# Kernel optimization log

Hardware: AMD Instinct MI355X
Metric: run time of the kernel (lower is better)

The kernel has to match this reference:

```python
import jax, jax.numpy as jnp
import numpy as np


def _lstm(x, Wih, Whh, bih, bhh):
    # x: (T, B, F); Wih: (4H, F); Whh: (4H, H); torch gate order i, f, g, o
    T, B, _ = x.shape
    H = Whh.shape[1]
    # precompute input projections for all timesteps (one big GEMM)
    xg = jnp.einsum('tbf,gf->tbg', x, Wih) + bih + bhh  # (T, B, 4H)

    def step(carry, gx):
        h, c = carry
        g = gx + h @ Whh.T  # (B, 4H)
        i, f, gg, o = jnp.split(g, 4, axis=-1)
        i = jax.nn.sigmoid(i)
        f = jax.nn.sigmoid(f)
        gg = jnp.tanh(gg)
        o = jax.nn.sigmoid(o)
        c = f * c + i * gg
        h = o * jnp.tanh(c)
        return (h, c), h

    h0 = jnp.zeros((B, H), x.dtype)
    (_, _), out = jax.lax.scan(step, (h0, h0), xg)
    return out  # (T, B, H)


def setup_inputs() -> dict:
    key = jax.random.key(0)
    ks = jax.random.split(key, 20)
    T, B, F = 1024, 512, 32
    H1, H2, H3 = 32, 8, 8  # lstm1 hidden=32, lstm2 hidden=8, lstm3 hidden=out_features=8
    p = 0.25
    s = 0.1  # weight init scale

    def mk_mask(k, h):
        keep = (jax.random.uniform(k, (B, h)) > p).astype(jnp.float32)
        return keep / (1.0 - p)

    return {
        'x': jax.random.normal(ks[0], (T, B, F), jnp.float32),
        'W_ih1': jax.random.normal(ks[1], (4 * H1, F)) * s,
        'W_hh1': jax.random.normal(ks[2], (4 * H1, H1)) * s,
        'b_ih1': jax.random.normal(ks[3], (4 * H1,)) * s,
        'b_hh1': jax.random.normal(ks[4], (4 * H1,)) * s,
        'W_ih2': jax.random.normal(ks[5], (4 * H2, H1)) * s,
        'W_hh2': jax.random.normal(ks[6], (4 * H2, H2)) * s,
        'b_ih2': jax.random.normal(ks[7], (4 * H2,)) * s,
        'b_hh2': jax.random.normal(ks[8], (4 * H2,)) * s,
        'W_ih3': jax.random.normal(ks[9], (4 * H3, H2)) * s,
        'W_hh3': jax.random.normal(ks[10], (4 * H3, H3)) * s,
        'b_ih3': jax.random.normal(ks[11], (4 * H3,)) * s,
        'b_hh3': jax.random.normal(ks[12], (4 * H3,)) * s,
        'mask1': mk_mask(ks[13], H1),
        'mask2': mk_mask(ks[14], H2),
        'mask3': mk_mask(ks[15], H3),
    }


def reference(x, W_ih1, W_hh1, b_ih1, b_hh1,
              W_ih2, W_hh2, b_ih2, b_hh2,
              W_ih3, W_hh3, b_ih3, b_hh3,
              mask1, mask2, mask3):
    # Locked (variational) output dropout: one mask per sequence, broadcast over time.
    out = _lstm(x, W_ih1, W_hh1, b_ih1, b_hh1) * mask1[None, :, :]
    out = _lstm(out, W_ih2, W_hh2, b_ih2, b_hh2) * mask2[None, :, :]
    out = _lstm(out, W_ih3, W_hh3, b_ih3, b_hh3) * mask3[None, :, :]
    return out  # (T, B, out_features)
```

## Files before the change

### kernel.cpp

```cpp
#include <hip/hip_runtime.h>


constexpr int T = 1024, B = 512, F = 32;
constexpr int H1 = 32, H2 = 8, H3 = 8;
constexpr int G1 = 4 * H1;
constexpr int HR = 128;
constexpr int XR = 64;
constexpr int OUT_STRIDE = B * H3;

typedef float f32x2 __attribute__((ext_vector_type(2)));
typedef unsigned int u32x2 __attribute__((ext_vector_type(2)));

#define PIN(v) asm volatile("" : "+v"(v))

#if __has_builtin(__builtin_amdgcn_rcpf)
#define RCPF(x) __builtin_amdgcn_rcpf(x)
#else
#define RCPF(x) (1.0f / (x))
#endif
#if __has_builtin(__builtin_amdgcn_exp2f)
#define EXP2F(x) __builtin_amdgcn_exp2f(x)
#else
#define EXP2F(x) exp2f(x)
#endif

#if __has_builtin(__builtin_amdgcn_permlane32_swap)
#define HAVE_PLSWAP 1
#else
#define HAVE_PLSWAP 0
#endif

#define SIG_CM (-1.4426950408889634f)

__device__ __forceinline__ void pkfma(f32x2& acc, f32x2 a, f32x2 b) {
    acc += a * b;
}

#define LDS_ACQ(p)    __hip_atomic_load((p), __ATOMIC_ACQUIRE, __HIP_MEMORY_SCOPE_WORKGROUP)
#define LDS_REL(p, v) __hip_atomic_store((p), (v), __ATOMIC_RELEASE, __HIP_MEMORY_SCOPE_WORKGROUP)
#define SPIN_UNTIL(EXPR)                                                       \
    do {                                                                       \
        int _g = 0;                                                            \
        while (!(EXPR)) {                                                      \
            __builtin_amdgcn_s_sleep(1);                                       \
            if (++_g > (1 << 23)) break;                                       \
        }                                                                      \
    } while (0)

__global__ __launch_bounds__(192, 1) void lstm3_fused_kernel(
    const float* __restrict__ x,
    const float* __restrict__ Wih1, const float* __restrict__ Whh1,
    const float* __restrict__ bih1, const float* __restrict__ bhh1,
    const float* __restrict__ Wih2, const float* __restrict__ Whh2,
    const float* __restrict__ bih2, const float* __restrict__ bhh2,
    const float* __restrict__ Wih3, const float* __restrict__ Whh3,
    const float* __restrict__ bih3, const float* __restrict__ bhh3,
    const float* __restrict__ mask1, const float* __restrict__ mask2,
    const float* __restrict__ mask3,
    float* __restrict__ out)
{
    const int tid = threadIdx.x;
    const int lane = tid & 63;
    const int wid = tid >> 6;
    const int b = blockIdx.x;

    __shared__ __align__(16) float h1ring[HR][H1];
    __shared__ __align__(16) float xgring[XR][G1];
    __shared__ __align__(16) float xstage[32][F];
    __shared__ __align__(16) float sh23[2][16];
    __shared__ int prog0, prog1, prog2;

    if (tid == 0) { prog0 = 0; prog1 = 0; prog2 = 0; }
    if (wid == 0 && lane < H1) h1ring[HR - 1][lane] = 0.f;
    if (wid == 1 && lane < 16) { sh23[0][lane] = 0.f; sh23[1][lane] = 0.f; }
    __syncthreads();

    if (wid == 2) {
        const float cmA = SIG_CM;
        const float cmB = (lane < 32) ? 2.0f * SIG_CM : SIG_CM;
        f32x2 wi0[16], wi1[16];
#pragma unroll
        for (int k = 0; k < 16; ++k) {
            wi0[k] = f32x2{Wih1[lane * F + 2 * k] * cmA, Wih1[lane * F + 2 * k + 1] * cmA};
            wi1[k] = f32x2{Wih1[(lane + 64) * F + 2 * k] * cmB, Wih1[(lane + 64) * F + 2 * k + 1] * cmB};
        }
        const float bias0 = (bih1[lane] + bhh1[lane]) * cmA;
        const float bias1 = (bih1[lane + 64] + bhh1[lane + 64]) * cmB;
#pragma unroll
        for (int k = 0; k < 16; ++k) { PIN(wi0[k]); PIN(wi1[k]); }

        const float4* x4 = (const float4*)x;
        float4* xr4 = (float4*)xstage;
        const int ttq = lane >> 3, ffq = lane & 7;

        float4 sA = x4[(size_t)(0 + ttq) * 4096 + b * 8 + ffq];
        float4 sB = x4[(size_t)(8 + ttq) * 4096 + b * 8 + ffq];
        xr4[(ttq & 31) * 8 + ffq] = sA;
        xr4[((8 + ttq) & 31) * 8 + ffq] = sB;
        sA = x4[(size_t)(16 + ttq) * 4096 + b * 8 + ffq];
        sB = x4[(size_t)(24 + ttq) * 4096 + b * 8 + ffq];

        for (int t = 0; t < T; ++t) {
            if ((t & 15) == 0) {
                const int need = t - 40;
                if (need > 0) SPIN_UNTIL(LDS_ACQ(&prog0) >= need);
                const int wt = t + 16;
                if (wt < T) {
                    xr4[((wt + ttq) & 31) * 8 + ffq] = sA;
                    xr4[((wt + 8 + ttq) & 31) * 8 + ffq] = sB;
                    const int lt = t + 32;
                    if (lt < T) {
                        sA = x4[(size_t)(lt + ttq) * 4096 + b * 8 + ffq];
                        sB = x4[(size_t)(lt + 8 + ttq) * 4096 + b * 8 + ffq];
                    }
                }
            }
            const float4* xp = (const float4*)xstage[t & 31];
            f32x2 aA = f32x2{bias0, 0.f}, aB = f32x2{0.f, 0.f};
            f32x2 cA = f32x2{bias1, 0.f}, cB = f32x2{0.f, 0.f};
#pragma unroll
            for (int q = 0; q < 8; ++q) {
                const float4 v = xp[q];
                const f32x2 lo = f32x2{v.x, v.y}, hi = f32x2{v.z, v.w};
                pkfma(aA, wi0[2 * q], lo); pkfma(aB, wi0[2 * q + 1], hi);
                pkfma(cA, wi1[2 * q], lo); pkfma(cB, wi1[2 * q + 1], hi);
            }
            const f32x2 sa = aA + aB, sc = cA + cB;
            xgring[t & (XR - 1)][lane] = sa.x + sa.y;
            xgring[t & (XR - 1)][lane + 64] = sc.x + sc.y;
            if ((t & 15) == 15) LDS_REL(&prog2, t + 1);
        }
    } else if (wid == 0) {
        const float s1d = 2.0f * SIG_CM;
        const float cm1 = (lane < 32) ? 2.0f * SIG_CM : SIG_CM;
        f32x2 w0[16], w1[16];
#pragma unroll
        for (int k = 0; k < 16; ++k) {
            w0[k] = f32x2{Whh1[lane * H1 + 2 * k] * SIG_CM, Whh1[lane * H1 + 2 * k + 1] * SIG_CM};
            w1[k] = f32x2{Whh1[(lane + 64) * H1 + 2 * k] * cm1, Whh1[(lane + 64) * H1 + 2 * k + 1] * cm1};
        }
#pragma unroll
        for (int k = 0; k < 16; ++k) { PIN(w0[k]); PIN(w1[k]); }
        const float ka1 = (lane < 32) ? (s1d + s1d) : 1.0f;
        const float kb1 = (lane < 32) ? -s1d : 0.0f;
        float c1s = 0.f;

        SPIN_UNTIL(LDS_ACQ(&prog2) >= ((34 < T) ? 34 : T));
        float pa = xgring[0][lane], pb = xgring[0][lane + 64];
        float na = xgring[1][lane], nb = xgring[1][lane + 64];

        for (int i = 0; i < T; ++i) {
            if ((i & 31) == 0 && i) {
                int tgt = i + 34; if (tgt > T) tgt = T;
                SPIN_UNTIL(LDS_ACQ(&prog2) >= tgt);
            }
            if ((i & 63) == 0 && i >= 64)
                SPIN_UNTIL(LDS_ACQ(&prog1) >= i - 48);

            const float4* h1p = (const float4*)h1ring[(i - 1) & (HR - 1)];
            f32x2 hp2[16];
#pragma unroll
            for (int q = 0; q < 8; ++q) {
                const float4 v = h1p[q];
                hp2[2 * q] = f32x2{v.x, v.y};
                hp2[2 * q + 1] = f32x2{v.z, v.w};
            }
            f32x2 A0 = f32x2{pa, 0.f}, A1 = f32x2{0.f, 0.f};
            f32x2 A2 = f32x2{0.f, 0.f}, A3 = f32x2{0.f, 0.f};
            f32x2 B0 = f32x2{pb, 0.f}, B1 = f32x2{0.f, 0.f};
            f32x2 B2 = f32x2{0.f, 0.f}, B3 = f32x2{0.f, 0.f};
#pragma unroll
            for (int d = 0; d < 4; ++d) {
                pkfma(A0, w0[0 + 4 * d], hp2[0 + 4 * d]);
                pkfma(A1, w0[1 + 4 * d], hp2[1 + 4 * d]);
                pkfma(A2, w0[2 + 4 * d], hp2[2 + 4 * d]);
                pkfma(A3, w0[3 + 4 * d], hp2[3 + 4 * d]);
                pkfma(B0, w1[0 + 4 * d], hp2[0 + 4 * d]);
                pkfma(B1, w1[1 + 4 * d], hp2[1 + 4 * d]);
                pkfma(B2, w1[2 + 4 * d], hp2[2 + 4 * d]);
                pkfma(B3, w1[3 + 4 * d], hp2[3 + 4 * d]);
            }
            const f32x2 SA = (A0 + A1) + (A2 + A3);
            const f32x2 SB = (B0 + B1) + (B2 + B3);
            const float a0s = SA.x + SA.y;
            const float a1s = SB.x + SB.y;
            const float g0 = RCPF(1.0f + EXP2F(a0s));
            const float g1 = fmaf(ka1, RCPF(1.0f + EXP2F(a1s)), kb1);
            pa = na; pb = nb;
            {
                int tn = i + 2; if (tn > T - 1) tn = T - 1;
                na = xgring[tn & (XR - 1)][lane];
                nb = xgring[tn & (XR - 1)][lane + 64];
            }
            float h1v;
#if HAVE_PLSWAP
            const u32x2 pif = __builtin_amdgcn_permlane32_swap(
                __float_as_uint(g0), __float_as_uint(g0), false, false);
            const u32x2 pgo = __builtin_amdgcn_permlane32_swap(
                __float_as_uint(g1), __float_as_uint(g1), false, false);
            const float iv = __uint_as_float(pif.x);
            const float fv = __uint_as_float(pif.y);
            const float gsv = __uint_as_float(pgo.x);
            const float ov = __uint_as_float(pgo.y);
            c1s = fmaf(fv, c1s, iv * gsv);
            const float rt = RCPF(1.0f + EXP2F(c1s));
            h1v = fmaf(ov + ov, rt, -ov);
#else
            const float fv = __shfl_xor(g0, 32);
            const float ov = __shfl_xor(g1, 32);
            c1s = fmaf(fv, c1s, g0 * g1);
            const float rt = RCPF(1.0f + EXP2F(c1s));
            h1v = fmaf(ov + ov, rt, -ov);
#endif
            if (lane < H1) h1ring[i & (HR - 1)][lane] = h1v;
            if ((i & 7) == 7) LDS_REL(&prog0, i + 1);
        }
    } else {
        const float sX = 2.0f * SIG_CM;
        const int r = lane & 31;
        const bool lower = (lane < 32);
        const int sec = r >> 3;
        const float cmX = (sec == 2) ? sX : SIG_CM;
        const float kaX = (sec == 2) ? (sX + sX) : 1.0f;
        const float kbX = (sec == 2) ? -sX : 0.0f;
        f32x2 wp[16];
        f32x2 wup[8];
        float biasX, m3;
        if (lower) {
#pragma unroll
            for (int k = 0; k < 16; ++k)
                wp[k] = f32x2{Wih2[r * H1 + 2 * k] * mask1[b * H1 + 2 * k] * cmX,
                              Wih2[r * H1 + 2 * k + 1] * mask1[b * H1 + 2 * k + 1] * cmX};
#pragma unroll
            for (int k = 0; k < 4; ++k)
                wup[k] = f32x2{Whh2[r * H2 + 2 * k] * cmX, Whh2[r * H2 + 2 * k + 1] * cmX};
#pragma unroll
            for (int k = 0; k < 4; ++k) wup[4 + k] = f32x2{0.f, 0.f};
            biasX = (bih2[r] + bhh2[r]) * cmX;
        } else {
#pragma unroll
            for (int k = 0; k < 16; ++k) wp[k] = f32x2{0.f, 0.f};
#pragma unroll
            for (int k = 0; k < 4; ++k)
                wup[k] = f32x2{Wih3[r * H2 + 2 * k] * mask2[b * H2 + 2 * k] * cmX,
                               Wih3[r * H2 + 2 * k + 1] * mask2[b * H2 + 2 * k + 1] * cmX};
#pragma unroll
            for (int k = 0; k < 4; ++k)
                wup[4 + k] = f32x2{Whh3[r * H3 + 2 * k] * cmX, Whh3[r * H3 + 2 * k + 1] * cmX};
            biasX = (bih3[r] + bhh3[r]) * cmX;
        }
        m3 = mask3[b * H3 + (lane & 7)];
        const int thresh = lower ? 1 : 2;
        const int gbase = (lane & 32) + (lane & 7);
        const int bx0 = 4 * (gbase + 0),  bx1 = 4 * (gbase + 8);
        const int bx2 = 4 * (gbase + 16), bx3 = 4 * (gbase + 24);
#pragma unroll
        for (int k = 0; k < 16; ++k) PIN(wp[k]);
#pragma unroll
        for (int k = 0; k < 8; ++k) PIN(wup[k]);

        float c23s = 0.f;
        f32x2 hq2[16];
        {
            const float4* hp0 = (const float4*)h1ring[HR - 1];
#pragma unroll
            for (int q = 0; q < 8; ++q) {
                const float4 v = hp0[q];
                hq2[2 * q] = f32x2{v.x, v.y};
                hq2[2 * q + 1] = f32x2{v.z, v.w};
            }
        }

        for (int i = 0; i <= T + 1; ++i) {
            if ((i & 7) == 0) {
                int tgt = i + 8; if (tgt > T) tgt = T;
                SPIN_UNTIL(LDS_ACQ(&prog0) >= tgt);
            }
            const int par = i & 1;
            const float4* up = (const float4*)sh23[par ^ 1];
            const float4 u0 = up[0], u1 = up[1], u2 = up[2], u3 = up[3];
            f32x2 S0 = f32x2{biasX, 0.f}, S1 = f32x2{0.f, 0.f};
            f32x2 S2 = f32x2{0.f, 0.f}, S3 = f32x2{0.f, 0.f};
#pragma unroll
            for (int d = 0; d < 4; ++d) {
                pkfma(S0, wp[0 + 4 * d], hq2[0 + 4 * d]);
                pkfma(S1, wp[1 + 4 * d], hq2[1 + 4 * d]);
                pkfma(S2, wp[2 + 4 * d], hq2[2 + 4 * d]);
                pkfma(S3, wp[3 + 4 * d], hq2[3 + 4 * d]);
            }
            f32x2 U0 = f32x2{0.f, 0.f}, U1 = f32x2{0.f, 0.f};
            f32x2 U2 = f32x2{0.f, 0.f}, U3 = f32x2{0.f, 0.f};
            pkfma(U0, wup[0], f32x2{u0.x, u0.y}); pkfma(U0, wup[4], f32x2{u2.x, u2.y});
            pkfma(U1, wup[1], f32x2{u0.z, u0.w}); pkfma(U1, wup[5], f32x2{u2.z, u2.w});
            pkfma(U2, wup[2], f32x2{u1.x, u1.y}); pkfma(U2, wup[6], f32x2{u3.x, u3.y});
            pkfma(U3, wup[3], f32x2{u1.z, u1.w}); pkfma(U3, wup[7], f32x2{u3.z, u3.w});
            const f32x2 ST = ((S0 + S1) + (S2 + S3)) + ((U0 + U1) + (U2 + U3));
            const float a23s = ST.x + ST.y;
            const float rv = fmaf(kaX, RCPF(1.0f + EXP2F(a23s)), kbX);
            float gi, gf, gg, go;
            asm volatile(
                "ds_bpermute_b32 %0, %4, %8\n\t"
                "ds_bpermute_b32 %1, %5, %8\n\t"
                "ds_bpermute_b32 %2, %6, %8\n\t"
                "ds_bpermute_b32 %3, %7, %8\n\t"
                "s_waitcnt lgkmcnt(0)"
                : "=&v"(gi), "=&v"(gf), "=&v"(gg), "=&v"(go)
                : "v"(bx0), "v"(bx1), "v"(bx2), "v"(bx3), "v"(rv)
                : "memory");
            {
                const float4* hp = (const float4*)h1ring[i & (HR - 1)];
#pragma unroll
                for (int q = 0; q < 8; ++q) {
                    const float4 v = hp[q];
                    hq2[2 * q] = f32x2{v.x, v.y};
                    hq2[2 * q + 1] = f32x2{v.z, v.w};
                }
            }
            c23s = (i >= thresh) ? fmaf(gf, c23s, gi * gg) : 0.0f;
            const float rt = RCPF(1.0f + EXP2F(c23s));
            const float hnew = fmaf(go + go, rt, -go);
            if (i >= 2 && (lane & 56) == 32)
                out[(size_t)(i - 2) * OUT_STRIDE + b * H3 + (lane & 7)] = hnew * m3;
            if ((lane & 24) == 0)
                sh23[par][(lane & 7) | ((lane & 32) >> 2)] = hnew;
            if ((i & 15) == 15) LDS_REL(&prog1, i + 1);
        }
    }
}

extern "C" void kernel_launch(void* const* d_in, const int* in_sizes, int n_in,
                              void* d_out, int out_size, void* d_ws, size_t ws_size,
                              hipStream_t stream) {
    (void)in_sizes; (void)n_in; (void)out_size; (void)d_ws; (void)ws_size;
    const float* x     = (const float*)d_in[0];
    const float* Wih1  = (const float*)d_in[1];
    const float* Whh1  = (const float*)d_in[2];
    const float* bih1  = (const float*)d_in[3];
    const float* bhh1  = (const float*)d_in[4];
    const float* Wih2  = (const float*)d_in[5];
    const float* Whh2  = (const float*)d_in[6];
    const float* bih2  = (const float*)d_in[7];
    const float* bhh2  = (const float*)d_in[8];
    const float* Wih3  = (const float*)d_in[9];
    const float* Whh3  = (const float*)d_in[10];
    const float* bih3  = (const float*)d_in[11];
    const float* bhh3  = (const float*)d_in[12];
    const float* mask1 = (const float*)d_in[13];
    const float* mask2 = (const float*)d_in[14];
    const float* mask3 = (const float*)d_in[15];
    float* out = (float*)d_out;

    lstm3_fused_kernel<<<dim3(B), dim3(192), 0, stream>>>(
        x, Wih1, Whh1, bih1, bhh1,
        Wih2, Whh2, bih2, bhh2,
        Wih3, Whh3, bih3, bhh3,
        mask1, mask2, mask3, out);
}
```

Measured before the change: 507.6 us.

## Process two batch sequences per block to interleave independent LSTM recurrences

Each block now handles two batch elements instead of one, with every wave running two independent recurrence chains interleaved in the same loop, and the grid halved. This is meant to hide the latency of the serial per-timestep dependency chain (LDS reads, exp/rcp, lane swaps, bpermute) by giving the scheduler independent work, and to halve the number of blocks on the device. It roughly doubles register pressure and removes the PIN register-pinning asm barriers, so spills or a worse schedule are possible. With 256 blocks on a part that has at least that many CUs, the per-block serial chain gets longer while total parallel width shrinks.

```diff
diff --git a/kernel.cpp b/kernel.cpp
--- a/kernel.cpp
+++ b/kernel.cpp
@@ -10,8 +10,6 @@
 
 typedef float f32x2 __attribute__((ext_vector_type(2)));
 typedef unsigned int u32x2 __attribute__((ext_vector_type(2)));
-
-#define PIN(v) asm volatile("" : "+v"(v))
 
 #if __has_builtin(__builtin_amdgcn_rcpf)
 #define RCPF(x) __builtin_amdgcn_rcpf(x)
@@ -62,17 +60,24 @@
     const int tid = threadIdx.x;
     const int lane = tid & 63;
     const int wid = tid >> 6;
-    const int b = blockIdx.x;
-
-    __shared__ __align__(16) float h1ring[HR][H1];
-    __shared__ __align__(16) float xgring[XR][G1];
-    __shared__ __align__(16) float xstage[32][F];
-    __shared__ __align__(16) float sh23[2][16];
+    const int b0 = 2 * blockIdx.x;
+    const int b1 = b0 + 1;
+
+    __shared__ __align__(16) float h1ring[2][HR][H1];
+    __shared__ __align__(16) float xgring[2][XR][G1];
+    __shared__ __align__(16) float xstage[2][32][F];
+    __shared__ __align__(16) float sh23[2][2][16];
     __shared__ int prog0, prog1, prog2;
 
     if (tid == 0) { prog0 = 0; prog1 = 0; prog2 = 0; }
-    if (wid == 0 && lane < H1) h1ring[HR - 1][lane] = 0.f;
-    if (wid == 1 && lane < 16) { sh23[0][lane] = 0.f; sh23[1][lane] = 0.f; }
+    if (wid == 0 && lane < H1) {
+        h1ring[0][HR - 1][lane] = 0.f;
+        h1ring[1][HR - 1][lane] = 0.f;
+    }
+    if (wid == 1 && lane < 16) {
+        sh23[0][0][lane] = 0.f; sh23[0][1][lane] = 0.f;
+        sh23[1][0][lane] = 0.f; sh23[1][1][lane] = 0.f;
+    }
     __syncthreads();
 
     if (wid == 2) {
@@ -86,19 +91,24 @@
         }
         const float bias0 = (bih1[lane] + bhh1[lane]) * cmA;
         const float bias1 = (bih1[lane + 64] + bhh1[lane + 64]) * cmB;
-#pragma unroll
-        for (int k = 0; k < 16; ++k) { PIN(wi0[k]); PIN(wi1[k]); }
 
         const float4* x4 = (const float4*)x;
-        float4* xr4 = (float4*)xstage;
+        float4* xr0 = (float4*)xstage[0];
+        float4* xr1 = (float4*)xstage[1];
         const int ttq = lane >> 3, ffq = lane & 7;
 
-        float4 sA = x4[(size_t)(0 + ttq) * 4096 + b * 8 + ffq];
-        float4 sB = x4[(size_t)(8 + ttq) * 4096 + b * 8 + ffq];
-        xr4[(ttq & 31) * 8 + ffq] = sA;
-        xr4[((8 + ttq) & 31) * 8 + ffq] = sB;
-        sA = x4[(size_t)(16 + ttq) * 4096 + b * 8 + ffq];
-        sB = x4[(size_t)(24 + ttq) * 4096 + b * 8 + ffq];
+        float4 sA0 = x4[(size_t)(0 + ttq) * 4096 + b0 * 8 + ffq];
+        float4 sB0 = x4[(size_t)(8 + ttq) * 4096 + b0 * 8 + ffq];
+        float4 sA1 = x4[(size_t)(0 + ttq) * 4096 + b1 * 8 + ffq];
+        float4 sB1 = x4[(size_t)(8 + ttq) * 4096 + b1 * 8 + ffq];
+        xr0[(ttq & 31) * 8 + ffq] = sA0;
+        xr0[((8 + ttq) & 31) * 8 + ffq] = sB0;
+        xr1[(ttq & 31) * 8 + ffq] = sA1;
+        xr1[((8 + ttq) & 31) * 8 + ffq] = sB1;
+        sA0 = x4[(size_t)(16 + ttq) * 4096 + b0 * 8 + ffq];
+        sB0 = x4[(size_t)(24 + ttq) * 4096 + b0 * 8 + ffq];
+        sA1 = x4[(size_t)(16 + ttq) * 4096 + b1 * 8 + ffq];
+        sB1 = x4[(size_t)(24 + ttq) * 4096 + b1 * 8 + ffq];
 
         for (int t = 0; t < T; ++t) {
             if ((t & 15) == 0) {
@@ -106,28 +116,41 @@
                 if (need > 0) SPIN_UNTIL(LDS_ACQ(&prog0) >= need);
                 const int wt = t + 16;
                 if (wt < T) {
-                    xr4[((wt + ttq) & 31) * 8 + ffq] = sA;
-                    xr4[((wt + 8 + ttq) & 31) * 8 + ffq] = sB;
+                    xr0[((wt + ttq) & 31) * 8 + ffq] = sA0;
+                    xr0[((wt + 8 + ttq) & 31) * 8 + ffq] = sB0;
+                    xr1[((wt + ttq) & 31) * 8 + ffq] = sA1;
+                    xr1[((wt + 8 + ttq) & 31) * 8 + ffq] = sB1;
                     const int lt = t + 32;
                     if (lt < T) {
-                        sA = x4[(size_t)(lt + ttq) * 4096 + b * 8 + ffq];
-                        sB = x4[(size_t)(lt + 8 + ttq) * 4096 + b * 8 + ffq];
+                        sA0 = x4[(size_t)(lt + ttq) * 4096 + b0 * 8 + ffq];
+                        sB0 = x4[(size_t)(lt + 8 + ttq) * 4096 + b0 * 8 + ffq];
+                        sA1 = x4[(size_t)(lt + ttq) * 4096 + b1 * 8 + ffq];
+                        sB1 = x4[(size_t)(lt + 8 + ttq) * 4096 + b1 * 8 + ffq];
                     }
                 }
             }
-            const float4* xp = (const float4*)xstage[t & 31];
-            f32x2 aA = f32x2{bias0, 0.f}, aB = f32x2{0.f, 0.f};
-            f32x2 cA = f32x2{bias1, 0.f}, cB = f32x2{0.f, 0.f};
+            const float4* xp0 = (const float4*)xstage[0][t & 31];
+            const float4* xp1 = (const float4*)xstage[1][t & 31];
+            f32x2 aA0 = f32x2{bias0, 0.f}, aB0 = f32x2{0.f, 0.f};
+            f32x2 cA0 = f32x2{bias1, 0.f}, cB0 = f32x2{0.f, 0.f};
+            f32x2 aA1 = f32x2{bias0, 0.f}, aB1 = f32x2{0.f, 0.f};
+            f32x2 cA1 = f32x2{bias1, 0.f}, cB1 = f32x2{0.f, 0.f};
 #pragma unroll
             for (int q = 0; q < 8; ++q) {
-                const float4 v = xp[q];
-                const f32x2 lo = f32x2{v.x, v.y}, hi = f32x2{v.z, v.w};
-                pkfma(aA, wi0[2 * q], lo); pkfma(aB, wi0[2 * q + 1], hi);
-                pkfma(cA, wi1[2 * q], lo); pkfma(cB, wi1[2 * q + 1], hi);
-            }
-            const f32x2 sa = aA + aB, sc = cA + cB;
-            xgring[t & (XR - 1)][lane] = sa.x + sa.y;
-            xgring[t & (XR - 1)][lane + 64] = sc.x + sc.y;
+                const float4 v0 = xp0[q], v1 = xp1[q];
+                const f32x2 lo0 = f32x2{v0.x, v0.y}, hi0 = f32x2{v0.z, v0.w};
+                const f32x2 lo1 = f32x2{v1.x, v1.y}, hi1 = f32x2{v1.z, v1.w};
+                pkfma(aA0, wi0[2 * q], lo0); pkfma(aB0, wi0[2 * q + 1], hi0);
+                pkfma(cA0, wi1[2 * q], lo0); pkfma(cB0, wi1[2 * q + 1], hi0);
+                pkfma(aA1, wi0[2 * q], lo1); pkfma(aB1, wi0[2 * q + 1], hi1);
+                pkfma(cA1, wi1[2 * q], lo1); pkfma(cB1, wi1[2 * q + 1], hi1);
+            }
+            const f32x2 sa0 = aA0 + aB0, sc0 = cA0 + cB0;
+            const f32x2 sa1 = aA1 + aB1, sc1 = cA1 + cB1;
+            xgring[0][t & (XR - 1)][lane] = sa0.x + sa0.y;
+            xgring[0][t & (XR - 1)][lane + 64] = sc0.x + sc0.y;
+            xgring[1][t & (XR - 1)][lane] = sa1.x + sa1.y;
+            xgring[1][t & (XR - 1)][lane + 64] = sc1.x + sc1.y;
             if ((t & 15) == 15) LDS_REL(&prog2, t + 1);
         }
     } else if (wid == 0) {
@@ -139,15 +162,15 @@
             w0[k] = f32x2{Whh1[lane * H1 + 2 * k] * SIG_CM, Whh1[lane * H1 + 2 * k + 1] * SIG_CM};
             w1[k] = f32x2{Whh1[(lane + 64) * H1 + 2 * k] * cm1, Whh1[(lane + 64) * H1 + 2 * k + 1] * cm1};
         }
-#pragma unroll
-        for (int k = 0; k < 16; ++k) { PIN(w0[k]); PIN(w1[k]); }
         const float ka1 = (lane < 32) ? (s1d + s1d) : 1.0f;
         const float kb1 = (lane < 32) ? -s1d : 0.0f;
-        float c1s = 0.f;
+        float c1s_0 = 0.f, c1s_1 = 0.f;
 
         SPIN_UNTIL(LDS_ACQ(&prog2) >= ((34 < T) ? 34 : T));
-        float pa = xgring[0][lane], pb = xgring[0][lane + 64];
-        float na = xgring[1][lane], nb = xgring[1][lane + 64];
+        float pa0 = xgring[0][0][lane], pb0 = xgring[0][0][lane + 64];
+        float na0 = xgring[0][1][lane], nb0 = xgring[0][1][lane + 64];
+        float pa1 = xgring[1][0][lane], pb1 = xgring[1][0][lane + 64];
+        float na1 = xgring[1][1][lane], nb1 = xgring[1][1][lane + 64];
 
         for (int i = 0; i < T; ++i) {
             if ((i & 31) == 0 && i) {
@@ -157,62 +180,111 @@
             if ((i & 63) == 0 && i >= 64)
                 SPIN_UNTIL(LDS_ACQ(&prog1) >= i - 48);
 
-            const float4* h1p = (const float4*)h1ring[(i - 1) & (HR - 1)];
-            f32x2 hp2[16];
+            const float4* h1p0 = (const float4*)h1ring[0][(i - 1) & (HR - 1)];
+            const float4* h1p1 = (const float4*)h1ring[1][(i - 1) & (HR - 1)];
+            f32x2 hp0[16], hp1[16];
 #pragma unroll
             for (int q = 0; q < 8; ++q) {
-                const float4 v = h1p[q];
-                hp2[2 * q] = f32x2{v.x, v.y};
-                hp2[2 * q + 1] = f32x2{v.z, v.w};
-            }
-            f32x2 A0 = f32x2{pa, 0.f}, A1 = f32x2{0.f, 0.f};
-            f32x2 A2 = f32x2{0.f, 0.f}, A3 = f32x2{0.f, 0.f};
-            f32x2 B0 = f32x2{pb, 0.f}, B1 = f32x2{0.f, 0.f};
-            f32x2 B2 = f32x2{0.f, 0.f}, B3 = f32x2{0.f, 0.f};
+                const float4 v = h1p0[q];
+                hp0[2 * q] = f32x2{v.x, v.y};
+                hp0[2 * q + 1] = f32x2{v.z, v.w};
+            }
+#pragma unroll
+            for (int q = 0; q < 8; ++q) {
+                const float4 v = h1p1[q];
+                hp1[2 * q] = f32x2{v.x, v.y};
+                hp1[2 * q + 1] = f32x2{v.z, v.w};
+            }
+            f32x2 A00 = f32x2{pa0, 0.f}, A01 = f32x2{0.f, 0.f};
+            f32x2 A02 = f32x2{0.f, 0.f}, A03 = f32x2{0.f, 0.f};
+            f32x2 B00 = f32x2{pb0, 0.f}, B01 = f32x2{0.f, 0.f};
+            f32x2 B02 = f32x2{0.f, 0.f}, B03 = f32x2{0.f, 0.f};
+            f32x2 A10 = f32x2{pa1, 0.f}, A11 = f32x2{0.f, 0.f};
+            f32x2 A12 = f32x2{0.f, 0.f}, A13 = f32x2{0.f, 0.f};
+            f32x2 B10 = f32x2{pb1, 0.f}, B11 = f32x2{0.f, 0.f};
+            f32x2 B12 = f32x2{0.f, 0.f}, B13 = f32x2{0.f, 0.f};
 #pragma unroll
             for (int d = 0; d < 4; ++d) {
-                pkfma(A0, w0[0 + 4 * d], hp2[0 + 4 * d]);
-                pkfma(A1, w0[1 + 4 * d], hp2[1 + 4 * d]);
-                pkfma(A2, w0[2 + 4 * d], hp2[2 + 4 * d]);
-                pkfma(A3, w0[3 + 4 * d], hp2[3 + 4 * d]);
-                pkfma(B0, w1[0 + 4 * d], hp2[0 + 4 * d]);
-                pkfma(B1, w1[1 + 4 * d], hp2[1 + 4 * d]);
-                pkfma(B2, w1[2 + 4 * d], hp2[2 + 4 * d]);
-                pkfma(B3, w1[3 + 4 * d], hp2[3 + 4 * d]);
-            }
-            const f32x2 SA = (A0 + A1) + (A2 + A3);
-            const f32x2 SB = (B0 + B1) + (B2 + B3);
-            const float a0s = SA.x + SA.y;
-            const float a1s = SB.x + SB.y;
-            const float g0 = RCPF(1.0f + EXP2F(a0s));
-            const float g1 = fmaf(ka1, RCPF(1.0f + EXP2F(a1s)), kb1);
-            pa = na; pb = nb;
+                pkfma(A00, w0[0 + 4 * d], hp0[0 + 4 * d]);
+                pkfma(A01, w0[1 + 4 * d], hp0[1 + 4 * d]);
+                pkfma(A02, w0[2 + 4 * d], hp0[2 + 4 * d]);
+                pkfma(A03, w0[3 + 4 * d], hp0[3 + 4 * d]);
+                pkfma(B00, w1[0 + 4 * d], hp0[0 + 4 * d]);
+                pkfma(B01, w1[1 + 4 * d], hp0[1 + 4 * d]);
+                pkfma(B02, w1[2 + 4 * d], hp0[2 + 4 * d]);
+                pkfma(B03, w1[3 + 4 * d], hp0[3 + 4 * d]);
+            }
+#pragma unroll
+            for (int d = 0; d < 4; ++d) {
+                pkfma(A10, w0[0 + 4 * d], hp1[0 + 4 * d]);
+                pkfma(A11, w0[1 + 4 * d], hp1[1 + 4 * d]);
+                pkfma(A12, w0[2 + 4 * d], hp1[2 + 4 * d]);
+                pkfma(A13, w0[3 + 4 * d], hp1[3 + 4 * d]);
+                pkfma(B10, w1[0 + 4 * d], hp1[0 + 4 * d]);
+                pkfma(B11, w1[1 + 4 * d], hp1[1 + 4 * d]);
+                pkfma(B12, w1[2 + 4 * d], hp1[2 + 4 * d]);
+                pkfma(B13, w1[3 + 4 * d], hp1[3 + 4 * d]);
+            }
+            const f32x2 SA0 = (A00 + A01) + (A02 + A03);
+            const f32x2 SB0 = (B00 + B01) + (B02 + B03);
+            const f32x2 SA1 = (A10 + A11) + (A12 + A13);
+            const f32x2 SB1 = (B10 + B11) + (B12 + B13);
+            const float g0_0 = RCPF(1.0f + EXP2F(SA0.x + SA0.y));
+            const float g1_0 = fmaf(ka1, RCPF(1.0f + EXP2F(SB0.x + SB0.y)), kb1);
+            const float g0_1 = RCPF(1.0f + EXP2F(SA1.x + SA1.y));
+            const float g1_1 = fmaf(ka1, RCPF(1.0f + EXP2F(SB1.x + SB1.y)), kb1);
+            pa0 = na0; pb0 = nb0; pa1 = na1; pb1 = nb1;
             {
                 int tn = i + 2; if (tn > T - 1) tn = T - 1;
-                na = xgring[tn & (XR - 1)][lane];
-                nb = xgring[tn & (XR - 1)][lane + 64];
-            }
-            float h1v;
+                na0 = xgring[0][tn & (XR - 1)][lane];
+                nb0 = xgring[0][tn & (XR - 1)][lane + 64];
+                na1 = xgring[1][tn & (XR - 1)][lane];
+                nb1 = xgring[1][tn & (XR - 1)][lane + 64];
+            }
+            float h1v0, h1v1;
 #if HAVE_PLSWAP
-            const u32x2 pif = __builtin_amdgcn_permlane32_swap(
-                __float_as_uint(g0), __float_as_uint(g0), false, false);
-            const u32x2 pgo = __builtin_amdgcn_permlane32_swap(
-                __float_as_uint(g1), __float_as_uint(g1), false, false);
-            const float iv = __uint_as_float(pif.x);
-            const float fv = __uint_as_float(pif.y);
-            const float gsv = __uint_as_float(pgo.x);
-            const float ov = __uint_as_float(pgo.y);
-            c1s = fmaf(fv, c1s, iv * gsv);
-            const float rt = RCPF(1.0f + EXP2F(c1s));
-            h1v = fmaf(ov + ov, rt, -ov);
+            {
+                const u32x2 pif = __builtin_amdgcn_permlane32_swap(
+                    __float_as_uint(g0_0), __float_as_uint(g0_0), false, false);
+                const u32x2 pgo = __builtin_amdgcn_permlane32_swap(
+                    __float_as_uint(g1_0), __float_as_uint(g1_0), false, false);
+                c1s_0 = fmaf(__uint_as_float(pif.y), c1s_0,
+                             __uint_as_float(pif.x) * __uint_as_float(pgo.x));
+                const float rt = RCPF(1.0f + EXP2F(c1s_0));
+                const float ov = __uint_as_float(pgo.y);
+                h1v0 = fmaf(ov + ov, rt, -ov);
+            }
+            {
+                const u32x2 pif = __builtin_amdgcn_permlane32_swap(
+                    __float_as_uint(g0_1), __float_as_uint(g0_1), false, false);
+                const u32x2 pgo = __builtin_amdgcn_permlane32_swap(
+                    __float_as_uint(g1_1), __float_as_uint(g1_1), false, false);
+                c1s_1 = fmaf(__uint_as_float(pif.y), c1s_1,
+                             __uint_as_float(pif.x) * __uint_as_float(pgo.x));
+                const float rt = RCPF(1.0f + EXP2F(c1s_1));
+                const float ov = __uint_as_float(pgo.y);
+                h1v1 = fmaf(ov + ov, rt, -ov);
+            }
 #else
-            const float fv = __shfl_xor(g0, 32);
-            const float ov = __shfl_xor(g1, 32);
-            c1s = fmaf(fv, c1s, g0 * g1);
-            const float rt = RCPF(1.0f + EXP2F(c1s));
-            h1v = fmaf(ov + ov, rt, -ov);
+            {
+                const float fv = __shfl_xor(g0_0, 32);
+                const float ov = __shfl_xor(g1_0, 32);
+                c1s_0 = fmaf(fv, c1s_0, g0_0 * g1_0);
+                const float rt = RCPF(1.0f + EXP2F(c1s_0));
+                h1v0 = fmaf(ov + ov, rt, -ov);
+            }
+            {
+                const float fv = __shfl_xor(g0_1, 32);
+                const float ov = __shfl_xor(g1_1, 32);
+                c1s_1 = fmaf(fv, c1s_1, g0_1 * g1_1);
+                const float rt = RCPF(1.0f + EXP2F(c1s_1));
+                h1v1 = fmaf(ov + ov, rt, -ov);
+            }
 #endif
-            if (lane < H1) h1ring[i & (HR - 1)][lane] = h1v;
+            if (lane < H1) {
+                h1ring[0][i & (HR - 1)][lane] = h1v0;
+                h1ring[1][i & (HR - 1)][lane] = h1v1;
+            }
             if ((i & 7) == 7) LDS_REL(&prog0, i + 1);
         }
     } else {
@@ -223,51 +295,63 @@
         const float cmX = (sec == 2) ? sX : SIG_CM;
         const float kaX = (sec == 2) ? (sX + sX) : 1.0f;
         const float kbX = (sec == 2) ? -sX : 0.0f;
-        f32x2 wp[16];
-        f32x2 wup[8];
-        float biasX, m3;
+        f32x2 wp0[16], wp1[16];
+        f32x2 wu0[8], wu1[8];
+        float biasX;
         if (lower) {
 #pragma unroll
-            for (int k = 0; k < 16; ++k)
-                wp[k] = f32x2{Wih2[r * H1 + 2 * k] * mask1[b * H1 + 2 * k] * cmX,
-                              Wih2[r * H1 + 2 * k + 1] * mask1[b * H1 + 2 * k + 1] * cmX};
-#pragma unroll
-            for (int k = 0; k < 4; ++k)
-                wup[k] = f32x2{Whh2[r * H2 + 2 * k] * cmX, Whh2[r * H2 + 2 * k + 1] * cmX};
-#pragma unroll
-            for (int k = 0; k < 4; ++k) wup[4 + k] = f32x2{0.f, 0.f};
+            for (int k = 0; k < 16; ++k) {
+                wp0[k] = f32x2{Wih2[r * H1 + 2 * k] * mask1[b0 * H1 + 2 * k] * cmX,
+                               Wih2[r * H1 + 2 * k + 1] * mask1[b0 * H1 + 2 * k + 1] * cmX};
+                wp1[k] = f32x2{Wih2[r * H1 + 2 * k] * mask1[b1 * H1 + 2 * k] * cmX,
+                               Wih2[r * H1 + 2 * k + 1] * mask1[b1 * H1 + 2 * k + 1] * cmX};
+            }
+#pragma unroll
+            for (int k = 0; k < 4; ++k) {
+                const f32x2 w = f32x2{Whh2[r * H2 + 2 * k] * cmX, Whh2[r * H2 + 2 * k + 1] * cmX};
+                wu0[k] = w; wu1[k] = w;
+            }
+#pragma unroll
+            for (int k = 0; k < 4; ++k) { wu0[4 + k] = f32x2{0.f, 0.f}; wu1[4 + k] = f32x2{0.f, 0.f}; }
             biasX = (bih2[r] + bhh2[r]) * cmX;
         } else {
 #pragma unroll
-            for (int k = 0; k < 16; ++k) wp[k] = f32x2{0.f, 0.f};
-#pragma unroll
-            for (int k = 0; k < 4; ++k)
-                wup[k] = f32x2{Wih3[r * H2 + 2 * k] * mask2[b * H2 + 2 * k] * cmX,
-                               Wih3[r * H2 + 2 * k + 1] * mask2[b * H2 + 2 * k + 1] * cmX};
-#pragma unroll
-            for (int k = 0; k < 4; ++k)
-                wup[4 + k] = f32x2{Whh3[r * H3 + 2 * k] * cmX, Whh3[r * H3 + 2 * k + 1] * cmX};
+            for (int k = 0; k < 16; ++k) { wp0[k] = f32x2{0.f, 0.f}; wp1[k] = f32x2{0.f, 0.f}; }
+#pragma unroll
+            for (int k = 0; k < 4; ++k) {
+                wu0[k] = f32x2{Wih3[r * H2 + 2 * k] * mask2[b0 * H2 + 2 * k] * cmX,
+                               Wih3[r * H2 + 2 * k + 1] * mask2[b0 * H2 + 2 * k + 1] * cmX};
+                wu1[k] = f32x2{Wih3[r * H2 + 2 * k] * mask2[b1 * H2 + 2 * k] * cmX,
+                               Wih3[r * H2 + 2 * k + 1] * mask2[b1 * H2 + 2 * k + 1] * cmX};
+            }
+#pragma unroll
+            for (int k = 0; k < 4; ++k) {
+                const f32x2 w = f32x2{Whh3[r * H3 + 2 * k] * cmX, Whh3[r * H3 + 2 * k + 1] * cmX};
+                wu0[4 + k] = w; wu1[4 + k] = w;
+            }
             biasX = (bih3[r] + bhh3[r]) * cmX;
         }
-        m3 = mask3[b * H3 + (lane & 7)];
+        const float m3_0 = mask3[b0 * H3 + (lane & 7)];
+        const float m3_1 = mask3[b1 * H3 + (lane & 7)];
         const int thresh = lower ? 1 : 2;
         const int gbase = (lane & 32) + (lane & 7);
         const int bx0 = 4 * (gbase + 0),  bx1 = 4 * (gbase + 8);
         const int bx2 = 4 * (gbase + 16), bx3 = 4 * (gbase + 24);
-#pragma unroll
-        for (int k = 0; k < 16; ++k) PIN(wp[k]);
-#pragma unroll
-        for (int k = 0; k < 8; ++k) PIN(wup[k]);
-
-        float c23s = 0.f;
-        f32x2 hq2[16];
+
+        float c23s_0 = 0.f, c23s_1 = 0.f;
+        f32x2 hq0[16], hq1[16];
         {
-            const float4* hp0 = (const float4*)h1ring[HR - 1];
+            const float4* p0 = (const float4*)h1ring[0][HR - 1];
+            const float4* p1 = (const float4*)h1ring[1][HR - 1];
 #pragma unroll
             for (int q = 0; q < 8; ++q) {
-                const float4 v = hp0[q];
-                hq2[2 * q] = f32x2{v.x, v.y};
-                hq2[2 * q + 1] = f32x2{v.z, v.w};
+                const float4 v = p0[q];
+                hq0[2 * q] = f32x2{v.x, v.y}; hq0[2 * q + 1] = f32x2{v.z, v.w};
+            }
+#pragma unroll
+            for (int q = 0; q < 8; ++q) {
+                const float4 v = p1[q];
+                hq1[2 * q] = f32x2{v.x, v.y}; hq1[2 * q + 1] = f32x2{v.z, v.w};
             }
         }
 
@@ -277,52 +361,85 @@
                 SPIN_UNTIL(LDS_ACQ(&prog0) >= tgt);
             }
             const int par = i & 1;
-            const float4* up = (const float4*)sh23[par ^ 1];
-            const float4 u0 = up[0], u1 = up[1], u2 = up[2], u3 = up[3];
-            f32x2 S0 = f32x2{biasX, 0.f}, S1 = f32x2{0.f, 0.f};
-            f32x2 S2 = f32x2{0.f, 0.f}, S3 = f32x2{0.f, 0.f};
+            const float4* up0 = (const float4*)sh23[0][par ^ 1];
+            const float4* up1 = (const float4*)sh23[1][par ^ 1];
+            const float4 u00 = up0[0], u01 = up0[1], u02 = up0[2], u03 = up0[3];
+            const float4 u10 = up1[0], u11 = up1[1], u12 = up1[2], u13 = up1[3];
+            f32x2 S00 = f32x2{biasX, 0.f}, S01 = f32x2{0.f, 0.f};
+            f32x2 S02 = f32x2{0.f, 0.f},  S03 = f32x2{0.f, 0.f};
+            f32x2 S10 = f32x2{biasX, 0.f}, S11 = f32x2{0.f, 0.f};
+            f32x2 S12 = f32x2{0.f, 0.f},  S13 = f32x2{0.f, 0.f};
 #pragma unroll
             for (int d = 0; d < 4; ++d) {
-                pkfma(S0, wp[0 + 4 * d], hq2[0 + 4 * d]);
-                pkfma(S1, wp[1 + 4 * d], hq2[1 + 4 * d]);
-                pkfma(S2, wp[2 + 4 * d], hq2[2 + 4 * d]);
-                pkfma(S3, wp[3 + 4 * d], hq2[3 + 4 * d]);
-            }
-            f32x2 U0 = f32x2{0.f, 0.f}, U1 = f32x2{0.f, 0.f};
-            f32x2 U2 = f32x2{0.f, 0.f}, U3 = f32x2{0.f, 0.f};
-            pkfma(U0, wup[0], f32x2{u0.x, u0.y}); pkfma(U0, wup[4], f32x2{u2.x, u2.y});
-            pkfma(U1, wup[1], f32x2{u0.z, u0.w}); pkfma(U1, wup[5], f32x2{u2.z, u2.w});
-            pkfma(U2, wup[2], f32x2{u1.x, u1.y}); pkfma(U2, wup[6], f32x2{u3.x, u3.y});
-            pkfma(U3, wup[3], f32x2{u1.z, u1.w}); pkfma(U3, wup[7], f32x2{u3.z, u3.w});
-            const f32x2 ST = ((S0 + S1) + (S2 + S3)) + ((U0 + U1) + (U2 + U3));
-            const float a23s = ST.x + ST.y;
-            const float rv = fmaf(kaX, RCPF(1.0f + EXP2F(a23s)), kbX);
-            float gi, gf, gg, go;
+                pkfma(S00, wp0[0 + 4 * d], hq0[0 + 4 * d]);
+                pkfma(S01, wp0[1 + 4 * d], hq0[1 + 4 * d]);
+                pkfma(S02, wp0[2 + 4 * d], hq0[2 + 4 * d]);
+                pkfma(S03, wp0[3 + 4 * d], hq0[3 + 4 * d]);
+                pkfma(S10, wp1[0 + 4 * d], hq1[0 + 4 * d]);
+                pkfma(S11, wp1[1 + 4 * d], hq1[1 + 4 * d]);
+                pkfma(S12, wp1[2 + 4 * d], hq1[2 + 4 * d]);
+                pkfma(S13, wp1[3 + 4 * d], hq1[3 + 4 * d]);
+            }
+            f32x2 U00 = f32x2{0.f, 0.f}, U01 = f32x2{0.f, 0.f};
+            f32x2 U02 = f32x2{0.f, 0.f}, U03 = f32x2{0.f, 0.f};
+            f32x2 U10 = f32x2{0.f, 0.f}, U11 = f32x2{0.f, 0.f};
+            f32x2 U12 = f32x2{0.f, 0.f}, U13 = f32x2{0.f, 0.f};
+            pkfma(U00, wu0[0], f32x2{u00.x, u00.y}); pkfma(U00, wu0[4], f32x2{u02.x, u02.y});
+            pkfma(U01, wu0[1], f32x2{u00.z, u00.w}); pkfma(U01, wu0[5], f32x2{u02.z, u02.w});
+            pkfma(U02, wu0[2], f32x2{u01.x, u01.y}); pkfma(U02, wu0[6], f32x2{u03.x, u03.y});
+            pkfma(U03, wu0[3], f32x2{u01.z, u01.w}); pkfma(U03, wu0[7], f32x2{u03.z, u03.w});
+            pkfma(U10, wu1[0], f32x2{u10.x, u10.y}); pkfma(U10, wu1[4], f32x2{u12.x, u12.y});
+            pkfma(U11, wu1[1], f32x2{u10.z, u10.w}); pkfma(U11, wu1[5], f32x2{u12.z, u12.w});
+            pkfma(U12, wu1[2], f32x2{u11.x, u11.y}); pkfma(U12, wu1[6], f32x2{u13.x, u13.y});
+            pkfma(U13, wu1[3], f32x2{u11.z, u11.w}); pkfma(U13, wu1[7], f32x2{u13.z, u13.w});
+            const f32x2 ST0 = ((S00 + S01) + (S02 + S03)) + ((U00 + U01) + (U02 + U03));
+            const f32x2 ST1 = ((S10 + S11) + (S12 + S13)) + ((U10 + U11) + (U12 + U13));
+            const float rv0 = fmaf(kaX, RCPF(1.0f + EXP2F(ST0.x + ST0.y)), kbX);
+            const float rv1 = fmaf(kaX, RCPF(1.0f + EXP2F(ST1.x + ST1.y)), kbX);
+            float gi0, gf0, gg0, go0, gi1, gf1, gg1, go1;
             asm volatile(
-                "ds_bpermute_b32 %0, %4, %8\n\t"
-                "ds_bpermute_b32 %1, %5, %8\n\t"
-                "ds_bpermute_b32 %2, %6, %8\n\t"
-                "ds_bpermute_b32 %3, %7, %8\n\t"
+                "ds_bpermute_b32 %0, %8, %12\n\t"
+                "ds_bpermute_b32 %1, %9, %12\n\t"
+                "ds_bpermute_b32 %2, %10, %12\n\t"
+                "ds_bpermute_b32 %3, %11, %12\n\t"
+                "ds_bpermute_b32 %4, %8, %13\n\t"
+                "ds_bpermute_b32 %5, %9, %13\n\t"
+                "ds_bpermute_b32 %6, %10, %13\n\t"
+                "ds_bpermute_b32 %7, %11, %13\n\t"
                 "s_waitcnt lgkmcnt(0)"
-                : "=&v"(gi), "=&v"(gf), "=&v"(gg), "=&v"(go)
-                : "v"(bx0), "v"(bx1), "v"(bx2), "v"(bx3), "v"(rv)
+                : "=&v"(gi0), "=&v"(gf0), "=&v"(gg0), "=&v"(go0),
+                  "=&v"(gi1), "=&v"(gf1), "=&v"(gg1), "=&v"(go1)
+                : "v"(bx0), "v"(bx1), "v"(bx2), "v"(bx3), "v"(rv0), "v"(rv1)
                 : "memory");
             {
-                const float4* hp = (const float4*)h1ring[i & (HR - 1)];
+                const float4* p0 = (const float4*)h1ring[0][i & (HR - 1)];
+                const float4* p1 = (const float4*)h1ring[1][i & (HR - 1)];
 #pragma unroll
                 for (int q = 0; q < 8; ++q) {
-                    const float4 v = hp[q];
-                    hq2[2 * q] = f32x2{v.x, v.y};
-                    hq2[2 * q + 1] = f32x2{v.z, v.w};
+                    const float4 v = p0[q];
+                    hq0[2 * q] = f32x2{v.x, v.y}; hq0[2 * q + 1] = f32x2{v.z, v.w};
                 }
-            }
-            c23s = (i >= thresh) ? fmaf(gf, c23s, gi * gg) : 0.0f;
-            const float rt = RCPF(1.0f + EXP2F(c23s));
-            const float hnew = fmaf(go + go, rt, -go);
-            if (i >= 2 && (lane & 56) == 32)
-                out[(size_t)(i - 2) * OUT_STRIDE + b * H3 + (lane & 7)] = hnew * m3;
-            if ((lane & 24) == 0)
-                sh23[par][(lane & 7) | ((lane & 32) >> 2)] = hnew;
+#pragma unroll
+                for (int q = 0; q < 8; ++q) {
+                    const float4 v = p1[q];
+                    hq1[2 * q] = f32x2{v.x, v.y}; hq1[2 * q + 1] = f32x2{v.z, v.w};
+                }
+            }
+            c23s_0 = (i >= thresh) ? fmaf(gf0, c23s_0, gi0 * gg0) : 0.0f;
+            c23s_1 = (i >= thresh) ? fmaf(gf1, c23s_1, gi1 * gg1) : 0.0f;
+            const float rt0 = RCPF(1.0f + EXP2F(c23s_0));
+            const float rt1 = RCPF(1.0f + EXP2F(c23s_1));
+            const float hn0 = fmaf(go0 + go0, rt0, -go0);
+            const float hn1 = fmaf(go1 + go1, rt1, -go1);
+            if (i >= 2 && (lane & 56) == 32) {
+                out[(size_t)(i - 2) * OUT_STRIDE + b0 * H3 + (lane & 7)] = hn0 * m3_0;
+                out[(size_t)(i - 2) * OUT_STRIDE + b1 * H3 + (lane & 7)] = hn1 * m3_1;
+            }
+            if ((lane & 24) == 0) {
+                const int si = (lane & 7) | ((lane & 32) >> 2);
+                sh23[0][par][si] = hn0;
+                sh23[1][par][si] = hn1;
+            }
             if ((i & 15) == 15) LDS_REL(&prog1, i + 1);
         }
     }
@@ -350,7 +467,7 @@
     const float* mask3 = (const float*)d_in[15];
     float* out = (float*)d_out;
 
-    lstm3_fused_kernel<<<dim3(B), dim3(192), 0, stream>>>(
+    lstm3_fused_kernel<<<dim3(B / 2), dim3(192), 0, stream>>>(
         x, Wih1, Whh1, bih1, bhh1,
         Wih2, Whh2, bih2, bhh2,
         Wih3, Whh3, bih3, bhh3,
```

Result: slower. 709.7 us (+39.8%).

## Broadcast half of layer-1 hidden state via DPP lane permutes instead of LDS

Applied to the files above, without the earlier changes.

In the layer-1 recurrent wave, each 16-lane group now gets its own half of the previous hidden state through DPP cross-lane permutes (xor patterns 1..15) straight from registers. Weights are pre-permuted to match. Only the other half is read back from the LDS ring, and that read is issued right after the store. The aim is to cut LDS round-trip latency and traffic on the serial per-timestep critical path. The change also drops the register-pinning asm barriers, the two-step xgring prefetch and the min-waves launch bound. These give the compiler more freedom but may raise register pressure or add exposed load latency.

```diff
diff --git a/kernel.cpp b/kernel.cpp
--- a/kernel.cpp
+++ b/kernel.cpp
@@ -11,8 +11,6 @@
 typedef float f32x2 __attribute__((ext_vector_type(2)));
 typedef unsigned int u32x2 __attribute__((ext_vector_type(2)));
 
-#define PIN(v) asm volatile("" : "+v"(v))
-
 #if __has_builtin(__builtin_amdgcn_rcpf)
 #define RCPF(x) __builtin_amdgcn_rcpf(x)
 #else
@@ -28,6 +26,11 @@
 #define HAVE_PLSWAP 1
 #else
 #define HAVE_PLSWAP 0
+#endif
+#if __has_builtin(__builtin_amdgcn_update_dpp)
+#define HAVE_DPP 1
+#else
+#define HAVE_DPP 0
 #endif
 
 #define SIG_CM (-1.4426950408889634f)
@@ -35,6 +38,14 @@
 __device__ __forceinline__ void pkfma(f32x2& acc, f32x2 a, f32x2 b) {
     acc += a * b;
 }
+
+#if HAVE_DPP
+template <int CTRL>
+__device__ __forceinline__ float dppf(float s) {
+    return __uint_as_float((unsigned)__builtin_amdgcn_update_dpp(
+        (int)__float_as_uint(s), (int)__float_as_uint(s), CTRL, 0xF, 0xF, false));
+}
+#endif
 
 #define LDS_ACQ(p)    __hip_atomic_load((p), __ATOMIC_ACQUIRE, __HIP_MEMORY_SCOPE_WORKGROUP)
 #define LDS_REL(p, v) __hip_atomic_store((p), (v), __ATOMIC_RELEASE, __HIP_MEMORY_SCOPE_WORKGROUP)
@@ -47,7 +58,7 @@
         }                                                                      \
     } while (0)
 
-__global__ __launch_bounds__(192, 1) void lstm3_fused_kernel(
+__global__ __launch_bounds__(192) void lstm3_fused_kernel(
     const float* __restrict__ x,
     const float* __restrict__ Wih1, const float* __restrict__ Whh1,
     const float* __restrict__ bih1, const float* __restrict__ bhh1,
@@ -86,8 +97,6 @@
         }
         const float bias0 = (bih1[lane] + bhh1[lane]) * cmA;
         const float bias1 = (bih1[lane + 64] + bhh1[lane + 64]) * cmB;
-#pragma unroll
-        for (int k = 0; k < 16; ++k) { PIN(wi0[k]); PIN(wi1[k]); }
 
         const float4* x4 = (const float4*)x;
         float4* xr4 = (float4*)xstage;
@@ -133,21 +142,35 @@
     } else if (wid == 0) {
         const float s1d = 2.0f * SIG_CM;
         const float cm1 = (lane < 32) ? 2.0f * SIG_CM : SIG_CM;
-        f32x2 w0[16], w1[16];
-#pragma unroll
-        for (int k = 0; k < 16; ++k) {
-            w0[k] = f32x2{Whh1[lane * H1 + 2 * k] * SIG_CM, Whh1[lane * H1 + 2 * k + 1] * SIG_CM};
-            w1[k] = f32x2{Whh1[(lane + 64) * H1 + 2 * k] * cm1, Whh1[(lane + 64) * H1 + 2 * k + 1] * cm1};
-        }
-#pragma unroll
-        for (int k = 0; k < 16; ++k) { PIN(w0[k]); PIN(w1[k]); }
+        const int o16 = lane & 15;
+        const int Gk = lane & 16;
+        const int GX = Gk ^ 16;
+        float w_own0[16], w_own1[16];
+#pragma unroll
+        for (int m = 0; m < 16; ++m) {
+            const int k = Gk | (o16 ^ m);
+            w_own0[m] = Whh1[lane * H1 + k] * SIG_CM;
+            w_own1[m] = Whh1[(lane + 64) * H1 + k] * cm1;
+        }
+        f32x2 wc0[8], wc1[8];
+#pragma unroll
+        for (int q = 0; q < 8; ++q) {
+            wc0[q] = f32x2{Whh1[lane * H1 + GX + 2 * q] * SIG_CM,
+                           Whh1[lane * H1 + GX + 2 * q + 1] * SIG_CM};
+            wc1[q] = f32x2{Whh1[(lane + 64) * H1 + GX + 2 * q] * cm1,
+                           Whh1[(lane + 64) * H1 + GX + 2 * q + 1] * cm1};
+        }
         const float ka1 = (lane < 32) ? (s1d + s1d) : 1.0f;
         const float kb1 = (lane < 32) ? -s1d : 0.0f;
         float c1s = 0.f;
+        float h1v = 0.f;
 
         SPIN_UNTIL(LDS_ACQ(&prog2) >= ((34 < T) ? 34 : T));
-        float pa = xgring[0][lane], pb = xgring[0][lane + 64];
-        float na = xgring[1][lane], nb = xgring[1][lane + 64];
+        float4 cr0, cr1, cr2, cr3;
+        {
+            const float4* cp = (const float4*)&h1ring[HR - 1][GX];
+            cr0 = cp[0]; cr1 = cp[1]; cr2 = cp[2]; cr3 = cp[3];
+        }
 
         for (int i = 0; i < T; ++i) {
             if ((i & 31) == 0 && i) {
@@ -157,42 +180,55 @@
             if ((i & 63) == 0 && i >= 64)
                 SPIN_UNTIL(LDS_ACQ(&prog1) >= i - 48);
 
-            const float4* h1p = (const float4*)h1ring[(i - 1) & (HR - 1)];
-            f32x2 hp2[16];
-#pragma unroll
-            for (int q = 0; q < 8; ++q) {
-                const float4 v = h1p[q];
-                hp2[2 * q] = f32x2{v.x, v.y};
-                hp2[2 * q + 1] = f32x2{v.z, v.w};
-            }
-            f32x2 A0 = f32x2{pa, 0.f}, A1 = f32x2{0.f, 0.f};
-            f32x2 A2 = f32x2{0.f, 0.f}, A3 = f32x2{0.f, 0.f};
-            f32x2 B0 = f32x2{pb, 0.f}, B1 = f32x2{0.f, 0.f};
-            f32x2 B2 = f32x2{0.f, 0.f}, B3 = f32x2{0.f, 0.f};
-#pragma unroll
-            for (int d = 0; d < 4; ++d) {
-                pkfma(A0, w0[0 + 4 * d], hp2[0 + 4 * d]);
-                pkfma(A1, w0[1 + 4 * d], hp2[1 + 4 * d]);
-                pkfma(A2, w0[2 + 4 * d], hp2[2 + 4 * d]);
-                pkfma(A3, w0[3 + 4 * d], hp2[3 + 4 * d]);
-                pkfma(B0, w1[0 + 4 * d], hp2[0 + 4 * d]);
-                pkfma(B1, w1[1 + 4 * d], hp2[1 + 4 * d]);
-                pkfma(B2, w1[2 + 4 * d], hp2[2 + 4 * d]);
-                pkfma(B3, w1[3 + 4 * d], hp2[3 + 4 * d]);
-            }
-            const f32x2 SA = (A0 + A1) + (A2 + A3);
-            const f32x2 SB = (B0 + B1) + (B2 + B3);
-            const float a0s = SA.x + SA.y;
-            const float a1s = SB.x + SB.y;
+            const float pa = xgring[i & (XR - 1)][lane];
+            const float pb = xgring[i & (XR - 1)][lane + 64];
+
+            float v[16];
+            v[0] = h1v;
+#if HAVE_DPP
+            v[1] = dppf<0xB1>(v[0]);
+            v[2] = dppf<0x4E>(v[0]);
+            v[3] = dppf<0x4E>(v[1]);
+#pragma unroll
+            for (int m = 0; m < 4; ++m)
+                v[4 + m] = dppf<0x1B>(dppf<0x141>(v[m]));
+#pragma unroll
+            for (int m = 0; m < 8; ++m)
+                v[8 + m] = dppf<0x141>(dppf<0x140>(v[m]));
+#else
+#pragma unroll
+            for (int m = 1; m < 16; ++m) v[m] = __shfl_xor(h1v, m);
+#endif
+            float a0A = 0.f, a0B = 0.f, a1A = 0.f, a1B = 0.f;
+#pragma unroll
+            for (int m = 0; m < 8; ++m) {
+                a0A = fmaf(v[m], w_own0[m], a0A);
+                a0B = fmaf(v[m + 8], w_own0[m + 8], a0B);
+                a1A = fmaf(v[m], w_own1[m], a1A);
+                a1B = fmaf(v[m + 8], w_own1[m + 8], a1B);
+            }
+            f32x2 C0 = f32x2{pa, 0.f}, C1 = f32x2{0.f, 0.f};
+            f32x2 D0 = f32x2{pb, 0.f}, D1 = f32x2{0.f, 0.f};
+            {
+                const f32x2 e0 = f32x2{cr0.x, cr0.y}, e1 = f32x2{cr0.z, cr0.w};
+                const f32x2 e2 = f32x2{cr1.x, cr1.y}, e3 = f32x2{cr1.z, cr1.w};
+                const f32x2 e4 = f32x2{cr2.x, cr2.y}, e5 = f32x2{cr2.z, cr2.w};
+                const f32x2 e6 = f32x2{cr3.x, cr3.y}, e7 = f32x2{cr3.z, cr3.w};
+                pkfma(C0, wc0[0], e0); pkfma(C1, wc0[1], e1);
+                pkfma(C0, wc0[2], e2); pkfma(C1, wc0[3], e3);
+                pkfma(C0, wc0[4], e4); pkfma(C1, wc0[5], e5);
+                pkfma(C0, wc0[6], e6); pkfma(C1, wc0[7], e7);
+                pkfma(D0, wc1[0], e0); pkfma(D1, wc1[1], e1);
+                pkfma(D0, wc1[2], e2); pkfma(D1, wc1[3], e3);
+                pkfma(D0, wc1[4], e4); pkfma(D1, wc1[5], e5);
+                pkfma(D0, wc1[6], e6); pkfma(D1, wc1[7], e7);
+            }
+            const f32x2 CS = C0 + C1, DS = D0 + D1;
+            const float a0s = ((a0A + a0B) + CS.x) + CS.y;
+            const float a1s = ((a1A + a1B) + DS.x) + DS.y;
             const float g0 = RCPF(1.0f + EXP2F(a0s));
             const float g1 = fmaf(ka1, RCPF(1.0f + EXP2F(a1s)), kb1);
-            pa = na; pb = nb;
-            {
-                int tn = i + 2; if (tn > T - 1) tn = T - 1;
-                na = xgring[tn & (XR - 1)][lane];
-                nb = xgring[tn & (XR - 1)][lane + 64];
-            }
-            float h1v;
+            float h1new;
 #if HAVE_PLSWAP
             const u32x2 pif = __builtin_amdgcn_permlane32_swap(
                 __float_as_uint(g0), __float_as_uint(g0), false, false);
@@ -204,15 +240,20 @@
             const float ov = __uint_as_float(pgo.y);
             c1s = fmaf(fv, c1s, iv * gsv);
             const float rt = RCPF(1.0f + EXP2F(c1s));
-            h1v = fmaf(ov + ov, rt, -ov);
+            h1new = fmaf(ov + ov, rt, -ov);
 #else
             const float fv = __shfl_xor(g0, 32);
             const float ov = __shfl_xor(g1, 32);
             c1s = fmaf(fv, c1s, g0 * g1);
             const float rt = RCPF(1.0f + EXP2F(c1s));
-            h1v = fmaf(ov + ov, rt, -ov);
-#endif
-            if (lane < H1) h1ring[i & (HR - 1)][lane] = h1v;
+            h1new = fmaf(ov + ov, rt, -ov);
+#endif
+            h1v = h1new;
+            if (lane < H1) h1ring[i & (HR - 1)][lane] = h1new;
+            {
+                const float4* cp = (const float4*)&h1ring[i & (HR - 1)][GX];
+                cr0 = cp[0]; cr1 = cp[1]; cr2 = cp[2]; cr3 = cp[3];
+            }
             if ((i & 7) == 7) LDS_REL(&prog0, i + 1);
         }
     } else {
@@ -254,10 +295,6 @@
         const int gbase = (lane & 32) + (lane & 7);
         const int bx0 = 4 * (gbase + 0),  bx1 = 4 * (gbase + 8);
         const int bx2 = 4 * (gbase + 16), bx3 = 4 * (gbase + 24);
-#pragma unroll
-        for (int k = 0; k < 16; ++k) PIN(wp[k]);
-#pragma unroll
-        for (int k = 0; k < 8; ++k) PIN(wup[k]);
 
         float c23s = 0.f;
         f32x2 hq2[16];
```

Result: slower. 598.3 us (+17.9%).
